# Kernel tuning notes

Hardware: AMD Instinct MI355X
Metric: run time of the kernel (lower is better)

Reference implementation:

```python
import jax, jax.numpy as jnp
import numpy as np

MAX_ITER = 15

def setup_inputs() -> dict:
    key = jax.random.key(0)
    k1, _ = jax.random.split(key)
    s = jax.random.normal(k1, (64, 1024, 1024), dtype=jnp.float32)
    temp = jnp.ones((1,), dtype=jnp.float32)
    return {"s": s, "temp": temp}

def reference(s, temp):
    # log-domain Sinkhorn (is_log=True, is_norm=True), max_iter=15
    s = s / temp  # temp broadcasts: [1] over [B, N, M]
    s = s - jax.scipy.special.logsumexp(s, axis=1, keepdims=True)
    for i in range(MAX_ITER):
        axis = 2 if (i % 2 == 0) else 1
        s = s - jax.scipy.special.logsumexp(s, axis=axis, keepdims=True)
    return jnp.exp(s)
```

## Files before the change

kernel.cpp:

```cpp
#include <hip/hip_runtime.h>
#include <stdint.h>

#define BB 64
#define NN 1024
#define MM 1024
#define CH 16

typedef unsigned short u16;
typedef __attribute__((ext_vector_type(8))) unsigned short ushort8v;

__device__ __forceinline__ float bf2f(u16 h) {
    union { uint32_t u; float f; } c; c.u = ((uint32_t)h) << 16; return c.f;
}
__device__ __forceinline__ u16 f2bf(float f) {
    union { float f; uint32_t u; } c; c.f = f;
    return (u16)((c.u + 0x7FFFu + ((c.u >> 16) & 1u)) >> 16);
}

__global__ __launch_bounds__(256) void k_convert(
    const float* __restrict__ s, const float* __restrict__ temp,
    u16* __restrict__ sbf, float* __restrict__ part)
{
    const int b     = blockIdx.x / CH;
    const int chunk = blockIdx.x % CH;
    const int col0  = threadIdx.x * 4;
    const float invt = 1.0f / temp[0];
    const int rows = NN / CH;
    const size_t base = ((size_t)b * NN + (size_t)chunk * rows) * MM + col0;
    const float* sp = s + base;
    u16* op = sbf + base;
    float S0 = 0.f, S1 = 0.f, S2 = 0.f, S3 = 0.f;
    for (int r = 0; r < rows; ++r) {
        float4 x = *reinterpret_cast<const float4*>(sp + (size_t)r * MM);
        float a0 = x.x * invt, a1 = x.y * invt, a2 = x.z * invt, a3 = x.w * invt;
        ushort4 o; o.x = f2bf(a0); o.y = f2bf(a1); o.z = f2bf(a2); o.w = f2bf(a3);
        *reinterpret_cast<ushort4*>(op + (size_t)r * MM) = o;
        S0 += __expf(a0); S1 += __expf(a1); S2 += __expf(a2); S3 += __expf(a3);
    }
    *reinterpret_cast<float4*>(part + ((size_t)b * CH + chunk) * MM + col0) =
        make_float4(S0, S1, S2, S3);
}

__global__ __launch_bounds__(256) void k_combine(
    const float* __restrict__ part, float* __restrict__ vout)
{
    const int idx = blockIdx.x * 256 + threadIdx.x;
    const int b = idx >> 10;
    const int j = idx & (MM - 1);
    float S = 0.f;
#pragma unroll
    for (int p = 0; p < CH; ++p) S += part[((size_t)b * CH + p) * MM + j];
    vout[idx] = __logf(S);
}

__global__ __launch_bounds__(256) void k_sweep(
    const u16* __restrict__ sbf, const float* __restrict__ v,
    float* __restrict__ part)
{
    __shared__ float sh[4][MM];
    const int b     = blockIdx.x / CH;
    const int chunk = blockIdx.x % CH;
    const int lane  = threadIdx.x & 63;
    const int wv    = threadIdx.x >> 6;
    const float* vp = v + (size_t)b * MM + lane * 16;
    float vv[16], ev[16];
    *reinterpret_cast<float4*>(&vv[0])  = *reinterpret_cast<const float4*>(vp);
    *reinterpret_cast<float4*>(&vv[4])  = *reinterpret_cast<const float4*>(vp + 4);
    *reinterpret_cast<float4*>(&vv[8])  = *reinterpret_cast<const float4*>(vp + 8);
    *reinterpret_cast<float4*>(&vv[12]) = *reinterpret_cast<const float4*>(vp + 12);
#pragma unroll
    for (int k = 0; k < 16; ++k) ev[k] = __expf(vv[k]);
    float Sc[16];
#pragma unroll
    for (int k = 0; k < 16; ++k) Sc[k] = 0.f;

    const int row0 = chunk * (NN / CH) + wv * 16;
    const u16* rp = sbf + ((size_t)b * NN + row0) * MM + lane * 16;
#pragma unroll 2
    for (int t = 0; t < 16; ++t) {
        ushort8v h0 = *reinterpret_cast<const ushort8v*>(rp + (size_t)t * MM);
        ushort8v h1 = *reinterpret_cast<const ushort8v*>(rp + (size_t)t * MM + 8);
        float te[16];
#pragma unroll
        for (int k = 0; k < 8; ++k) te[k]     = __expf(bf2f(h0[k]) - vv[k]);
#pragma unroll
        for (int k = 0; k < 8; ++k) te[8 + k] = __expf(bf2f(h1[k]) - vv[8 + k]);
        float Sr = 0.f;
#pragma unroll
        for (int k = 0; k < 16; ++k) Sr += te[k];
#pragma unroll
        for (int off = 32; off >= 1; off >>= 1) Sr += __shfl_xor(Sr, off);
        const float w = __builtin_amdgcn_rcpf(Sr);
#pragma unroll
        for (int k = 0; k < 16; ++k) Sc[k] = fmaf(te[k], ev[k] * w, Sc[k]);
    }
#pragma unroll
    for (int q = 0; q < 4; ++q)
        *reinterpret_cast<float4*>(&sh[wv][lane * 16 + q * 4]) =
            *reinterpret_cast<float4*>(&Sc[q * 4]);
    __syncthreads();
    const int c0 = threadIdx.x * 4;
    float4 a0 = *reinterpret_cast<float4*>(&sh[0][c0]);
    float4 a1 = *reinterpret_cast<float4*>(&sh[1][c0]);
    float4 a2 = *reinterpret_cast<float4*>(&sh[2][c0]);
    float4 a3 = *reinterpret_cast<float4*>(&sh[3][c0]);
    float4 r;
    r.x = (a0.x + a1.x) + (a2.x + a3.x);
    r.y = (a0.y + a1.y) + (a2.y + a3.y);
    r.z = (a0.z + a1.z) + (a2.z + a3.z);
    r.w = (a0.w + a1.w) + (a2.w + a3.w);
    *reinterpret_cast<float4*>(part + ((size_t)b * CH + chunk) * MM + c0) = r;
}

__global__ __launch_bounds__(256) void k_final(
    const float* __restrict__ s, const float* __restrict__ temp,
    const float* __restrict__ v, float* __restrict__ out)
{
    const int lane = threadIdx.x & 63;
    const int row  = blockIdx.x * 4 + (threadIdx.x >> 6);
    const int b    = row >> 10;
    const float invt = 1.0f / temp[0];
    const float* sp = s + (size_t)row * MM + lane * 16;
    const float* vp = v + (size_t)b * MM + lane * 16;
    float e[16];
    float S = 0.f;
#pragma unroll
    for (int q = 0; q < 4; ++q) {
        float4 xs = *reinterpret_cast<const float4*>(sp + q * 4);
        float4 vs = *reinterpret_cast<const float4*>(vp + q * 4);
        e[4*q+0] = __expf(xs.x * invt - vs.x);
        e[4*q+1] = __expf(xs.y * invt - vs.y);
        e[4*q+2] = __expf(xs.z * invt - vs.z);
        e[4*q+3] = __expf(xs.w * invt - vs.w);
        S += (e[4*q+0] + e[4*q+1]) + (e[4*q+2] + e[4*q+3]);
    }
#pragma unroll
    for (int off = 32; off >= 1; off >>= 1) S += __shfl_xor(S, off);
    const float w = 1.0f / S;
    float* op = out + (size_t)row * MM + lane * 16;
#pragma unroll
    for (int q = 0; q < 4; ++q) {
        float4 o;
        o.x = e[4*q+0] * w; o.y = e[4*q+1] * w;
        o.z = e[4*q+2] * w; o.w = e[4*q+3] * w;
        *reinterpret_cast<float4*>(op + q * 4) = o;
    }
}

extern "C" void kernel_launch(void* const* d_in, const int* in_sizes, int n_in,
                              void* d_out, int out_size, void* d_ws, size_t ws_size,
                              hipStream_t stream) {
    (void)in_sizes; (void)n_in; (void)out_size; (void)ws_size;
    const float* s    = (const float*)d_in[0];
    const float* temp = (const float*)d_in[1];
    float* out = (float*)d_out;

    u16*   sbf  = (u16*)d_out;
    float* part = (float*)((char*)d_out + ((size_t)BB * NN * MM) * sizeof(u16));
    float* v    = (float*)d_ws;

    dim3 blk(256);
    k_convert<<<dim3(BB * CH), blk, 0, stream>>>(s, temp, sbf, part);
    k_combine<<<dim3(BB * MM / 256), blk, 0, stream>>>(part, v);
    for (int p = 0; p < 7; ++p) {
        k_sweep<<<dim3(BB * CH), blk, 0, stream>>>(sbf, v, part);
        k_combine<<<dim3(BB * MM / 256), blk, 0, stream>>>(part, v);
    }
    k_final<<<dim3(BB * NN / 4), blk, 0, stream>>>(s, temp, v, out);
}
```

Baseline: 387.3 us.

## Fuse all Sinkhorn passes into one persistent kernel with per-batch atomic barriers

Replaces the seventeen separate launches (convert, combine, seven sweep and combine pairs, final) with a single persistent kernel of 512 blocks, eight per batch. Blocks in a batch synchronise through spin-wait atomic counters, and the column combine is done redundantly inside each block. A grid-wide barrier guards the final pass, which overwrites the bf16 scratch held in the output buffer. The aim is to remove launch gaps and the separate combine kernels, and non-temporal loads and stores are added for the fp32 streams. The risk is that spin barriers deadlock if not all blocks are co-resident, and eight blocks per batch give less parallelism than sixteen.

After: 1.388 ms. +258.4%, slower.

```diff
diff --git a/kernel.cpp b/kernel.cpp
--- a/kernel.cpp
+++ b/kernel.cpp
@@ -4,10 +4,14 @@
 #define BB 64
 #define NN 1024
 #define MM 1024
-#define CH 16
+#define BPB 8
+#define RPB (NN / BPB)
+#define RPW (RPB / 4)
+#define NBLK (BB * BPB)
 
 typedef unsigned short u16;
 typedef __attribute__((ext_vector_type(8))) unsigned short ushort8v;
+typedef __attribute__((ext_vector_type(4))) float f32x4;
 
 __device__ __forceinline__ float bf2f(u16 h) {
     union { uint32_t u; float f; } c; c.u = ((uint32_t)h) << 16; return c.f;
@@ -17,133 +21,190 @@
     return (u16)((c.u + 0x7FFFu + ((c.u >> 16) & 1u)) >> 16);
 }
 
-__global__ __launch_bounds__(256) void k_convert(
+__device__ __forceinline__ void bat_bar(int* ctr, int target) {
+    __syncthreads();
+    if (threadIdx.x == 0) {
+        __threadfence();
+        __hip_atomic_fetch_add(ctr, 1, __ATOMIC_RELEASE, __HIP_MEMORY_SCOPE_AGENT);
+        while (__hip_atomic_load(ctr, __ATOMIC_ACQUIRE, __HIP_MEMORY_SCOPE_AGENT) < target)
+            __builtin_amdgcn_s_sleep(2);
+    }
+    __syncthreads();
+    __threadfence();
+}
+
+__global__ void k_init(int* c) {
+    if (threadIdx.x <= BB) c[threadIdx.x * 16] = 0;
+}
+
+__global__ __launch_bounds__(256, 4) void k_sink(
     const float* __restrict__ s, const float* __restrict__ temp,
-    u16* __restrict__ sbf, float* __restrict__ part)
-{
-    const int b     = blockIdx.x / CH;
-    const int chunk = blockIdx.x % CH;
-    const int col0  = threadIdx.x * 4;
-    const float invt = 1.0f / temp[0];
-    const int rows = NN / CH;
-    const size_t base = ((size_t)b * NN + (size_t)chunk * rows) * MM + col0;
-    const float* sp = s + base;
-    u16* op = sbf + base;
-    float S0 = 0.f, S1 = 0.f, S2 = 0.f, S3 = 0.f;
-    for (int r = 0; r < rows; ++r) {
-        float4 x = *reinterpret_cast<const float4*>(sp + (size_t)r * MM);
-        float a0 = x.x * invt, a1 = x.y * invt, a2 = x.z * invt, a3 = x.w * invt;
-        ushort4 o; o.x = f2bf(a0); o.y = f2bf(a1); o.z = f2bf(a2); o.w = f2bf(a3);
-        *reinterpret_cast<ushort4*>(op + (size_t)r * MM) = o;
-        S0 += __expf(a0); S1 += __expf(a1); S2 += __expf(a2); S3 += __expf(a3);
-    }
-    *reinterpret_cast<float4*>(part + ((size_t)b * CH + chunk) * MM + col0) =
-        make_float4(S0, S1, S2, S3);
-}
-
-__global__ __launch_bounds__(256) void k_combine(
-    const float* __restrict__ part, float* __restrict__ vout)
-{
-    const int idx = blockIdx.x * 256 + threadIdx.x;
-    const int b = idx >> 10;
-    const int j = idx & (MM - 1);
-    float S = 0.f;
-#pragma unroll
-    for (int p = 0; p < CH; ++p) S += part[((size_t)b * CH + p) * MM + j];
-    vout[idx] = __logf(S);
-}
-
-__global__ __launch_bounds__(256) void k_sweep(
-    const u16* __restrict__ sbf, const float* __restrict__ v,
-    float* __restrict__ part)
+    u16* __restrict__ sbf, float* __restrict__ p0, float* __restrict__ p1,
+    float* __restrict__ out, int* __restrict__ bar, int* __restrict__ gbar)
 {
     __shared__ float sh[4][MM];
-    const int b     = blockIdx.x / CH;
-    const int chunk = blockIdx.x % CH;
-    const int lane  = threadIdx.x & 63;
-    const int wv    = threadIdx.x >> 6;
-    const float* vp = v + (size_t)b * MM + lane * 16;
-    float vv[16], ev[16];
-    *reinterpret_cast<float4*>(&vv[0])  = *reinterpret_cast<const float4*>(vp);
-    *reinterpret_cast<float4*>(&vv[4])  = *reinterpret_cast<const float4*>(vp + 4);
-    *reinterpret_cast<float4*>(&vv[8])  = *reinterpret_cast<const float4*>(vp + 8);
-    *reinterpret_cast<float4*>(&vv[12]) = *reinterpret_cast<const float4*>(vp + 12);
-#pragma unroll
-    for (int k = 0; k < 16; ++k) ev[k] = __expf(vv[k]);
-    float Sc[16];
-#pragma unroll
-    for (int k = 0; k < 16; ++k) Sc[k] = 0.f;
-
-    const int row0 = chunk * (NN / CH) + wv * 16;
-    const u16* rp = sbf + ((size_t)b * NN + row0) * MM + lane * 16;
+    const int b     = blockIdx.x >> 3;
+    const int chunk = blockIdx.x & 7;
+    const int tid   = threadIdx.x;
+    const int lane  = tid & 63;
+    const int wv    = tid >> 6;
+    const float invt = 1.0f / temp[0];
+    int* mybar = bar + b * 16;
+
+    {
+        const size_t base = ((size_t)b * NN + chunk * RPB) * MM + tid * 4;
+        const float* sp = s + base;
+        u16* op = sbf + base;
+        float S0 = 0.f, S1 = 0.f, S2 = 0.f, S3 = 0.f;
+        for (int r = 0; r < RPB; ++r) {
+            f32x4 x = __builtin_nontemporal_load(
+                reinterpret_cast<const f32x4*>(sp + (size_t)r * MM));
+            float a0 = x.x * invt, a1 = x.y * invt, a2 = x.z * invt, a3 = x.w * invt;
+            ushort4 o; o.x = f2bf(a0); o.y = f2bf(a1); o.z = f2bf(a2); o.w = f2bf(a3);
+            *reinterpret_cast<ushort4*>(op + (size_t)r * MM) = o;
+            S0 += __expf(a0); S1 += __expf(a1); S2 += __expf(a2); S3 += __expf(a3);
+        }
+        *reinterpret_cast<float4*>(p0 + ((size_t)b * BPB + chunk) * MM + tid * 4)
+            = make_float4(S0, S1, S2, S3);
+    }
+    bat_bar(mybar, BPB * 1);
+
+    const float* psrc = p0;
+    float*       pdst = p1;
+    const u16* rp = sbf + ((size_t)b * NN + chunk * RPB + wv * RPW) * MM + lane * 16;
+
+    for (int p = 0; p < 7; ++p) {
+        {
+            const int c0 = tid * 4;
+            float4 acc = make_float4(0.f, 0.f, 0.f, 0.f);
+#pragma unroll
+            for (int q = 0; q < BPB; ++q) {
+                float4 pr = *reinterpret_cast<const float4*>(
+                    psrc + ((size_t)b * BPB + q) * MM + c0);
+                acc.x += pr.x; acc.y += pr.y; acc.z += pr.z; acc.w += pr.w;
+            }
+            float4 lv;
+            lv.x = __logf(acc.x); lv.y = __logf(acc.y);
+            lv.z = __logf(acc.z); lv.w = __logf(acc.w);
+            *reinterpret_cast<float4*>(&sh[0][c0]) = lv;
+            *reinterpret_cast<float4*>(&sh[1][c0]) = acc;
+        }
+        __syncthreads();
+        float vv[16], ev[16];
+#pragma unroll
+        for (int q = 0; q < 4; ++q) {
+            *reinterpret_cast<float4*>(&vv[q*4]) =
+                *reinterpret_cast<const float4*>(&sh[0][lane*16 + q*4]);
+            *reinterpret_cast<float4*>(&ev[q*4]) =
+                *reinterpret_cast<const float4*>(&sh[1][lane*16 + q*4]);
+        }
+        __syncthreads();
+
+        float Sc[16];
+#pragma unroll
+        for (int k = 0; k < 16; ++k) Sc[k] = 0.f;
 #pragma unroll 2
-    for (int t = 0; t < 16; ++t) {
-        ushort8v h0 = *reinterpret_cast<const ushort8v*>(rp + (size_t)t * MM);
-        ushort8v h1 = *reinterpret_cast<const ushort8v*>(rp + (size_t)t * MM + 8);
-        float te[16];
-#pragma unroll
-        for (int k = 0; k < 8; ++k) te[k]     = __expf(bf2f(h0[k]) - vv[k]);
-#pragma unroll
-        for (int k = 0; k < 8; ++k) te[8 + k] = __expf(bf2f(h1[k]) - vv[8 + k]);
-        float Sr = 0.f;
-#pragma unroll
-        for (int k = 0; k < 16; ++k) Sr += te[k];
-#pragma unroll
-        for (int off = 32; off >= 1; off >>= 1) Sr += __shfl_xor(Sr, off);
-        const float w = __builtin_amdgcn_rcpf(Sr);
-#pragma unroll
-        for (int k = 0; k < 16; ++k) Sc[k] = fmaf(te[k], ev[k] * w, Sc[k]);
-    }
+        for (int t = 0; t < RPW; ++t) {
+            ushort8v h0 = *reinterpret_cast<const ushort8v*>(rp + (size_t)t * MM);
+            ushort8v h1 = *reinterpret_cast<const ushort8v*>(rp + (size_t)t * MM + 8);
+            float te[16];
+#pragma unroll
+            for (int k = 0; k < 8; ++k) te[k]     = __expf(bf2f(h0[k]) - vv[k]);
+#pragma unroll
+            for (int k = 0; k < 8; ++k) te[8 + k] = __expf(bf2f(h1[k]) - vv[8 + k]);
+            float Sr = 0.f;
+#pragma unroll
+            for (int k = 0; k < 16; ++k) Sr += te[k];
+#pragma unroll
+            for (int off = 32; off >= 1; off >>= 1) Sr += __shfl_xor(Sr, off);
+            const float w = __builtin_amdgcn_rcpf(Sr);
+#pragma unroll
+            for (int k = 0; k < 16; ++k) Sc[k] = fmaf(te[k], w, Sc[k]);
+        }
+#pragma unroll
+        for (int k = 0; k < 16; ++k) Sc[k] *= ev[k];
+
+#pragma unroll
+        for (int q = 0; q < 4; ++q)
+            *reinterpret_cast<float4*>(&sh[wv][lane*16 + q*4]) =
+                *reinterpret_cast<float4*>(&Sc[q*4]);
+        __syncthreads();
+        {
+            const int c0 = tid * 4;
+            float4 a0 = *reinterpret_cast<float4*>(&sh[0][c0]);
+            float4 a1 = *reinterpret_cast<float4*>(&sh[1][c0]);
+            float4 a2 = *reinterpret_cast<float4*>(&sh[2][c0]);
+            float4 a3 = *reinterpret_cast<float4*>(&sh[3][c0]);
+            float4 r;
+            r.x = (a0.x + a1.x) + (a2.x + a3.x);
+            r.y = (a0.y + a1.y) + (a2.y + a3.y);
+            r.z = (a0.z + a1.z) + (a2.z + a3.z);
+            r.w = (a0.w + a1.w) + (a2.w + a3.w);
+            *reinterpret_cast<float4*>(pdst + ((size_t)b * BPB + chunk) * MM + c0) = r;
+        }
+        bat_bar(mybar, BPB * (2 + p));
+        const float* t2 = psrc; psrc = pdst; pdst = (float*)t2;
+    }
+
+    {
+        const int c0 = tid * 4;
+        float4 acc = make_float4(0.f, 0.f, 0.f, 0.f);
+#pragma unroll
+        for (int q = 0; q < BPB; ++q) {
+            float4 pr = *reinterpret_cast<const float4*>(
+                psrc + ((size_t)b * BPB + q) * MM + c0);
+            acc.x += pr.x; acc.y += pr.y; acc.z += pr.z; acc.w += pr.w;
+        }
+        float4 lv;
+        lv.x = __logf(acc.x); lv.y = __logf(acc.y);
+        lv.z = __logf(acc.z); lv.w = __logf(acc.w);
+        *reinterpret_cast<float4*>(&sh[0][c0]) = lv;
+    }
+    __syncthreads();
+    float vv[16];
 #pragma unroll
     for (int q = 0; q < 4; ++q)
-        *reinterpret_cast<float4*>(&sh[wv][lane * 16 + q * 4]) =
-            *reinterpret_cast<float4*>(&Sc[q * 4]);
-    __syncthreads();
-    const int c0 = threadIdx.x * 4;
-    float4 a0 = *reinterpret_cast<float4*>(&sh[0][c0]);
-    float4 a1 = *reinterpret_cast<float4*>(&sh[1][c0]);
-    float4 a2 = *reinterpret_cast<float4*>(&sh[2][c0]);
-    float4 a3 = *reinterpret_cast<float4*>(&sh[3][c0]);
-    float4 r;
-    r.x = (a0.x + a1.x) + (a2.x + a3.x);
-    r.y = (a0.y + a1.y) + (a2.y + a3.y);
-    r.z = (a0.z + a1.z) + (a2.z + a3.z);
-    r.w = (a0.w + a1.w) + (a2.w + a3.w);
-    *reinterpret_cast<float4*>(part + ((size_t)b * CH + chunk) * MM + c0) = r;
-}
-
-__global__ __launch_bounds__(256) void k_final(
-    const float* __restrict__ s, const float* __restrict__ temp,
-    const float* __restrict__ v, float* __restrict__ out)
-{
-    const int lane = threadIdx.x & 63;
-    const int row  = blockIdx.x * 4 + (threadIdx.x >> 6);
-    const int b    = row >> 10;
-    const float invt = 1.0f / temp[0];
-    const float* sp = s + (size_t)row * MM + lane * 16;
-    const float* vp = v + (size_t)b * MM + lane * 16;
-    float e[16];
-    float S = 0.f;
-#pragma unroll
-    for (int q = 0; q < 4; ++q) {
-        float4 xs = *reinterpret_cast<const float4*>(sp + q * 4);
-        float4 vs = *reinterpret_cast<const float4*>(vp + q * 4);
-        e[4*q+0] = __expf(xs.x * invt - vs.x);
-        e[4*q+1] = __expf(xs.y * invt - vs.y);
-        e[4*q+2] = __expf(xs.z * invt - vs.z);
-        e[4*q+3] = __expf(xs.w * invt - vs.w);
-        S += (e[4*q+0] + e[4*q+1]) + (e[4*q+2] + e[4*q+3]);
-    }
-#pragma unroll
-    for (int off = 32; off >= 1; off >>= 1) S += __shfl_xor(S, off);
-    const float w = 1.0f / S;
-    float* op = out + (size_t)row * MM + lane * 16;
-#pragma unroll
-    for (int q = 0; q < 4; ++q) {
-        float4 o;
-        o.x = e[4*q+0] * w; o.y = e[4*q+1] * w;
-        o.z = e[4*q+2] * w; o.w = e[4*q+3] * w;
-        *reinterpret_cast<float4*>(op + q * 4) = o;
+        *reinterpret_cast<float4*>(&vv[q*4]) =
+            *reinterpret_cast<const float4*>(&sh[0][lane*16 + q*4]);
+
+    __syncthreads();
+    if (tid == 0) {
+        __threadfence();
+        __hip_atomic_fetch_add(gbar, 1, __ATOMIC_RELEASE, __HIP_MEMORY_SCOPE_AGENT);
+        while (__hip_atomic_load(gbar, __ATOMIC_ACQUIRE, __HIP_MEMORY_SCOPE_AGENT) < NBLK)
+            __builtin_amdgcn_s_sleep(2);
+    }
+    __syncthreads();
+    __threadfence();
+
+    {
+        const float* sp = s   + ((size_t)b * NN + chunk * RPB + wv * RPW) * MM + lane * 16;
+        float*       op = out + ((size_t)b * NN + chunk * RPB + wv * RPW) * MM + lane * 16;
+#pragma unroll 2
+        for (int t = 0; t < RPW; ++t) {
+            float e[16]; float S = 0.f;
+#pragma unroll
+            for (int q = 0; q < 4; ++q) {
+                f32x4 xs = __builtin_nontemporal_load(
+                    reinterpret_cast<const f32x4*>(sp + (size_t)t * MM + q * 4));
+                e[q*4+0] = __expf(xs.x * invt - vv[q*4+0]);
+                e[q*4+1] = __expf(xs.y * invt - vv[q*4+1]);
+                e[q*4+2] = __expf(xs.z * invt - vv[q*4+2]);
+                e[q*4+3] = __expf(xs.w * invt - vv[q*4+3]);
+                S += (e[q*4+0] + e[q*4+1]) + (e[q*4+2] + e[q*4+3]);
+            }
+#pragma unroll
+            for (int off = 32; off >= 1; off >>= 1) S += __shfl_xor(S, off);
+            const float w = 1.0f / S;
+#pragma unroll
+            for (int q = 0; q < 4; ++q) {
+                f32x4 o;
+                o.x = e[q*4+0] * w; o.y = e[q*4+1] * w;
+                o.z = e[q*4+2] * w; o.w = e[q*4+3] * w;
+                __builtin_nontemporal_store(o,
+                    reinterpret_cast<f32x4*>(op + (size_t)t * MM + q * 4));
+            }
+        }
     }
 }
 
@@ -155,16 +216,12 @@
     const float* temp = (const float*)d_in[1];
     float* out = (float*)d_out;
 
-    u16*   sbf  = (u16*)d_out;
-    float* part = (float*)((char*)d_out + ((size_t)BB * NN * MM) * sizeof(u16));
-    float* v    = (float*)d_ws;
-
-    dim3 blk(256);
-    k_convert<<<dim3(BB * CH), blk, 0, stream>>>(s, temp, sbf, part);
-    k_combine<<<dim3(BB * MM / 256), blk, 0, stream>>>(part, v);
-    for (int p = 0; p < 7; ++p) {
-        k_sweep<<<dim3(BB * CH), blk, 0, stream>>>(sbf, v, part);
-        k_combine<<<dim3(BB * MM / 256), blk, 0, stream>>>(part, v);
-    }
-    k_final<<<dim3(BB * NN / 4), blk, 0, stream>>>(s, temp, v, out);
-}
+    u16*   sbf = (u16*)d_out;
+    float* p0  = (float*)((char*)d_out + (size_t)BB * NN * MM * sizeof(u16));
+    float* p1  = p0 + (size_t)BB * BPB * MM;
+    int*   bar  = (int*)d_ws;
+    int*   gbar = bar + BB * 16;
+
+    k_init<<<1, 128, 0, stream>>>(bar);
+    k_sink<<<dim3(NBLK), dim3(256), 0, stream>>>(s, temp, sbf, p0, p1, out, bar, gbar);
+}
```

## Fuse partial-sum combine into sweep kernel with ping-pong partial buffers

Applied to the files above, without the earlier changes.

Each sweep block now reduces the 16 chunk partials for its batch itself, computes log and keeps the raw sum as exp(v), and double-buffers the partial arrays so the separate combine launches between sweeps disappear. The per-element ev multiply is also hoisted out of the row loop and applied once at the end. This removes seven small kernel launches and their dependency stalls, at the cost of every one of the 16 blocks per batch redundantly reading all partials.

Measured after the change: 398.8 us. 3.0% more time.

```diff
diff --git a/kernel.cpp b/kernel.cpp
--- a/kernel.cpp
+++ b/kernel.cpp
@@ -41,35 +41,43 @@
         make_float4(S0, S1, S2, S3);
 }
 
-__global__ __launch_bounds__(256) void k_combine(
-    const float* __restrict__ part, float* __restrict__ vout)
-{
-    const int idx = blockIdx.x * 256 + threadIdx.x;
-    const int b = idx >> 10;
-    const int j = idx & (MM - 1);
-    float S = 0.f;
-#pragma unroll
-    for (int p = 0; p < CH; ++p) S += part[((size_t)b * CH + p) * MM + j];
-    vout[idx] = __logf(S);
-}
-
 __global__ __launch_bounds__(256) void k_sweep(
-    const u16* __restrict__ sbf, const float* __restrict__ v,
-    float* __restrict__ part)
+    const u16* __restrict__ sbf, const float* __restrict__ psrc,
+    float* __restrict__ pdst)
 {
     __shared__ float sh[4][MM];
     const int b     = blockIdx.x / CH;
     const int chunk = blockIdx.x % CH;
-    const int lane  = threadIdx.x & 63;
-    const int wv    = threadIdx.x >> 6;
-    const float* vp = v + (size_t)b * MM + lane * 16;
+    const int tid   = threadIdx.x;
+    const int lane  = tid & 63;
+    const int wv    = tid >> 6;
+
+    {
+        const int c0 = tid * 4;
+        float4 acc = make_float4(0.f, 0.f, 0.f, 0.f);
+#pragma unroll
+        for (int q = 0; q < CH; ++q) {
+            float4 pr = *reinterpret_cast<const float4*>(
+                psrc + ((size_t)b * CH + q) * MM + c0);
+            acc.x += pr.x; acc.y += pr.y; acc.z += pr.z; acc.w += pr.w;
+        }
+        float4 lv;
+        lv.x = __logf(acc.x); lv.y = __logf(acc.y);
+        lv.z = __logf(acc.z); lv.w = __logf(acc.w);
+        *reinterpret_cast<float4*>(&sh[0][c0]) = lv;
+        *reinterpret_cast<float4*>(&sh[1][c0]) = acc;
+    }
+    __syncthreads();
     float vv[16], ev[16];
-    *reinterpret_cast<float4*>(&vv[0])  = *reinterpret_cast<const float4*>(vp);
-    *reinterpret_cast<float4*>(&vv[4])  = *reinterpret_cast<const float4*>(vp + 4);
-    *reinterpret_cast<float4*>(&vv[8])  = *reinterpret_cast<const float4*>(vp + 8);
-    *reinterpret_cast<float4*>(&vv[12]) = *reinterpret_cast<const float4*>(vp + 12);
 #pragma unroll
-    for (int k = 0; k < 16; ++k) ev[k] = __expf(vv[k]);
+    for (int q = 0; q < 4; ++q) {
+        *reinterpret_cast<float4*>(&vv[q*4]) =
+            *reinterpret_cast<const float4*>(&sh[0][lane*16 + q*4]);
+        *reinterpret_cast<float4*>(&ev[q*4]) =
+            *reinterpret_cast<const float4*>(&sh[1][lane*16 + q*4]);
+    }
+    __syncthreads();
+
     float Sc[16];
 #pragma unroll
     for (int k = 0; k < 16; ++k) Sc[k] = 0.f;
@@ -92,24 +100,41 @@
         for (int off = 32; off >= 1; off >>= 1) Sr += __shfl_xor(Sr, off);
         const float w = __builtin_amdgcn_rcpf(Sr);
 #pragma unroll
-        for (int k = 0; k < 16; ++k) Sc[k] = fmaf(te[k], ev[k] * w, Sc[k]);
+        for (int k = 0; k < 16; ++k) Sc[k] = fmaf(te[k], w, Sc[k]);
     }
 #pragma unroll
+    for (int k = 0; k < 16; ++k) Sc[k] *= ev[k];
+
+#pragma unroll
     for (int q = 0; q < 4; ++q)
-        *reinterpret_cast<float4*>(&sh[wv][lane * 16 + q * 4]) =
-            *reinterpret_cast<float4*>(&Sc[q * 4]);
+        *reinterpret_cast<float4*>(&sh[wv][lane*16 + q*4]) =
+            *reinterpret_cast<float4*>(&Sc[q*4]);
     __syncthreads();
-    const int c0 = threadIdx.x * 4;
-    float4 a0 = *reinterpret_cast<float4*>(&sh[0][c0]);
-    float4 a1 = *reinterpret_cast<float4*>(&sh[1][c0]);
-    float4 a2 = *reinterpret_cast<float4*>(&sh[2][c0]);
-    float4 a3 = *reinterpret_cast<float4*>(&sh[3][c0]);
-    float4 r;
-    r.x = (a0.x + a1.x) + (a2.x + a3.x);
-    r.y = (a0.y + a1.y) + (a2.y + a3.y);
-    r.z = (a0.z + a1.z) + (a2.z + a3.z);
-    r.w = (a0.w + a1.w) + (a2.w + a3.w);
-    *reinterpret_cast<float4*>(part + ((size_t)b * CH + chunk) * MM + c0) = r;
+    {
+        const int c0 = tid * 4;
+        float4 a0 = *reinterpret_cast<float4*>(&sh[0][c0]);
+        float4 a1 = *reinterpret_cast<float4*>(&sh[1][c0]);
+        float4 a2 = *reinterpret_cast<float4*>(&sh[2][c0]);
+        float4 a3 = *reinterpret_cast<float4*>(&sh[3][c0]);
+        float4 r;
+        r.x = (a0.x + a1.x) + (a2.x + a3.x);
+        r.y = (a0.y + a1.y) + (a2.y + a3.y);
+        r.z = (a0.z + a1.z) + (a2.z + a3.z);
+        r.w = (a0.w + a1.w) + (a2.w + a3.w);
+        *reinterpret_cast<float4*>(pdst + ((size_t)b * CH + chunk) * MM + c0) = r;
+    }
+}
+
+__global__ __launch_bounds__(256) void k_combine(
+    const float* __restrict__ part, float* __restrict__ vout)
+{
+    const int idx = blockIdx.x * 256 + threadIdx.x;
+    const int b = idx >> 10;
+    const int j = idx & (MM - 1);
+    float S = 0.f;
+#pragma unroll
+    for (int p = 0; p < CH; ++p) S += part[((size_t)b * CH + p) * MM + j];
+    vout[idx] = __logf(S);
 }
 
 __global__ __launch_bounds__(256) void k_final(
@@ -128,11 +153,11 @@
     for (int q = 0; q < 4; ++q) {
         float4 xs = *reinterpret_cast<const float4*>(sp + q * 4);
         float4 vs = *reinterpret_cast<const float4*>(vp + q * 4);
-        e[4*q+0] = __expf(xs.x * invt - vs.x);
-        e[4*q+1] = __expf(xs.y * invt - vs.y);
-        e[4*q+2] = __expf(xs.z * invt - vs.z);
-        e[4*q+3] = __expf(xs.w * invt - vs.w);
-        S += (e[4*q+0] + e[4*q+1]) + (e[4*q+2] + e[4*q+3]);
+        e[q*4+0] = __expf(xs.x * invt - vs.x);
+        e[q*4+1] = __expf(xs.y * invt - vs.y);
+        e[q*4+2] = __expf(xs.z * invt - vs.z);
+        e[q*4+3] = __expf(xs.w * invt - vs.w);
+        S += (e[q*4+0] + e[q*4+1]) + (e[q*4+2] + e[q*4+3]);
     }
 #pragma unroll
     for (int off = 32; off >= 1; off >>= 1) S += __shfl_xor(S, off);
@@ -141,8 +166,8 @@
 #pragma unroll
     for (int q = 0; q < 4; ++q) {
         float4 o;
-        o.x = e[4*q+0] * w; o.y = e[4*q+1] * w;
-        o.z = e[4*q+2] * w; o.w = e[4*q+3] * w;
+        o.x = e[q*4+0] * w; o.y = e[q*4+1] * w;
+        o.z = e[q*4+2] * w; o.w = e[q*4+3] * w;
         *reinterpret_cast<float4*>(op + q * 4) = o;
     }
 }
@@ -155,16 +180,18 @@
     const float* temp = (const float*)d_in[1];
     float* out = (float*)d_out;
 
-    u16*   sbf  = (u16*)d_out;
-    float* part = (float*)((char*)d_out + ((size_t)BB * NN * MM) * sizeof(u16));
-    float* v    = (float*)d_ws;
+    u16*   sbf = (u16*)d_out;
+    float* p0  = (float*)((char*)d_out + (size_t)BB * NN * MM * sizeof(u16));
+    float* p1  = p0 + (size_t)BB * CH * MM;
+    float* v   = (float*)d_ws;
 
     dim3 blk(256);
-    k_convert<<<dim3(BB * CH), blk, 0, stream>>>(s, temp, sbf, part);
-    k_combine<<<dim3(BB * MM / 256), blk, 0, stream>>>(part, v);
+    k_convert<<<dim3(BB * CH), blk, 0, stream>>>(s, temp, sbf, p0);
+    const float* ps = p0; float* pd = p1;
     for (int p = 0; p < 7; ++p) {
-        k_sweep<<<dim3(BB * CH), blk, 0, stream>>>(sbf, v, part);
-        k_combine<<<dim3(BB * MM / 256), blk, 0, stream>>>(part, v);
+        k_sweep<<<dim3(BB * CH), blk, 0, stream>>>(sbf, ps, pd);
+        const float* t2 = ps; ps = pd; pd = (float*)t2;
     }
+    k_combine<<<dim3(BB * MM / 256), blk, 0, stream>>>(ps, v);
     k_final<<<dim3(BB * NN / 4), blk, 0, stream>>>(s, temp, v, out);
 }
```
